# Performance work log

Hardware: AMD Instinct MI355X
Metric: run time of the kernel (lower is better)

## Reference

```python
import jax, jax.numpy as jnp
import numpy as np

N_HEAD = 8
D_ATTN = 64
D_MODEL = 512


def setup_inputs() -> dict:
    key = jax.random.key(0)
    ks = jax.random.split(key, 12)
    B, S = 2, 2048
    inp = {
        "input": jax.random.normal(ks[0], (B, S, D_MODEL), dtype=jnp.float32),
        "top": jax.random.normal(ks[1], (B, S, S, 16), dtype=jnp.float32),
        # learned params (Linear: y = x @ W.T + b)
        "top_w": jax.random.normal(ks[2], (1, 16), dtype=jnp.float32) * 0.25,
        "top_b": jnp.zeros((1,), dtype=jnp.float32),
        "wq": jax.random.normal(ks[3], (N_HEAD * D_ATTN, D_MODEL), dtype=jnp.float32) * 0.02,
        "bq": jnp.zeros((N_HEAD * D_ATTN,), dtype=jnp.float32),
        "wk": jax.random.normal(ks[4], (N_HEAD * D_ATTN, D_MODEL), dtype=jnp.float32) * 0.02,
        "bk": jnp.zeros((N_HEAD * D_ATTN,), dtype=jnp.float32),
        "wv": jax.random.normal(ks[5], (N_HEAD * D_ATTN, D_MODEL), dtype=jnp.float32) * 0.02,
        "bv": jnp.zeros((N_HEAD * D_ATTN,), dtype=jnp.float32),
        "wo": jax.random.normal(ks[6], (D_MODEL, N_HEAD * D_ATTN), dtype=jnp.float32) * 0.02,
        "bo": jnp.zeros((D_MODEL,), dtype=jnp.float32),
    }
    return inp


def reference(input, top, top_w, top_b, wq, bq, wk, bk, wv, bv, wo, bo):
    B, S, _ = input.shape
    # pairwise topological bias: [B,S,S,16] @ [16,1] -> [B,S,S]
    bias = (jnp.einsum('bstf,f->bst', top, top_w[0]) + top_b[0])  # [B,S,S]
    bias = bias[:, None, :, :]  # broadcast over heads: [B,1,S,S]

    def proj(w, b):
        # [B,S,D] -> [B,H,S,d]
        return (input @ w.T + b).reshape(B, S, N_HEAD, D_ATTN).transpose(0, 2, 1, 3)

    Q, K, V = proj(wq, bq), proj(wk, bk), proj(wv, bv)
    scores = jnp.einsum('bhqd,bhkd->bhqk', Q, K) / jnp.sqrt(jnp.float32(D_ATTN))
    attn = jax.nn.softmax(scores + bias, axis=-1)
    O = jnp.einsum('bhqk,bhkd->bhqd', attn, V)  # [B,H,S,d]
    O = O.transpose(0, 2, 1, 3).reshape(B, S, N_HEAD * D_ATTN)
    return O @ wo.T + bo
```

## Files before the change

kernel.cpp:

```cpp
#include <hip/hip_runtime.h>
#include <math.h>

#define S_LEN 2048
#define BATCH 2
#define NH 8
#define DH 64
#define DM 512

typedef __attribute__((ext_vector_type(8))) short short8;
typedef __attribute__((ext_vector_type(4))) float floatx4;

__device__ __forceinline__ unsigned short f2bf(float f) {
  union { float f; unsigned u; } v; v.f = f;
  unsigned r = v.u + 0x7FFFu + ((v.u >> 16) & 1u);
  return (unsigned short)(r >> 16);
}

__global__ __launch_bounds__(256) void cvt_f32_bf16(const float* __restrict__ src,
                                                    unsigned short* __restrict__ dst, int n4) {
  int i = blockIdx.x * blockDim.x + threadIdx.x;
  if (i < n4) {
    float4 f = ((const float4*)src)[i];
    ushort4 o;
    o.x = f2bf(f.x); o.y = f2bf(f.y); o.z = f2bf(f.z); o.w = f2bf(f.w);
    ((ushort4*)dst)[i] = o;
  }
}

__global__ __launch_bounds__(256) void bias_topo(const float* __restrict__ top,
                                                 const float* __restrict__ top_w,
                                                 const float* __restrict__ top_b,
                                                 float* __restrict__ bias) {
  size_t e = (size_t)blockIdx.x * blockDim.x + threadIdx.x;
  const float4* t = (const float4*)(top + e * 16);
  const float4* w = (const float4*)top_w;
  float acc = top_b[0];
#pragma unroll
  for (int j = 0; j < 4; j++) {
    float4 tv = t[j]; float4 wv = w[j];
    acc += tv.x * wv.x + tv.y * wv.y + tv.z * wv.z + tv.w * wv.w;
  }
  bias[e] = acc;
}

__global__ __launch_bounds__(256) void gemm_bt(const unsigned short* __restrict__ A,
                                               const unsigned short* __restrict__ W,
                                               const float* __restrict__ bias,
                                               void* __restrict__ out, int mode, float scale) {
  __shared__ unsigned short As[64][72];
  __shared__ unsigned short Ws[64][72];
  const int m0 = blockIdx.x * 64, n0 = blockIdx.y * 64;
  const int tid = threadIdx.x;
  const int w = tid >> 6, l = tid & 63;
  const int lr = l & 15, lg = l >> 4;

  floatx4 acc[4];
#pragma unroll
  for (int nb = 0; nb < 4; nb++)
#pragma unroll
    for (int i = 0; i < 4; i++) acc[nb][i] = 0.f;

  const int srow = tid >> 2;
  const int sseg = (tid & 3) * 16;

  for (int k0 = 0; k0 < 512; k0 += 64) {
    const unsigned short* ap = A + (size_t)(m0 + srow) * 512 + k0 + sseg;
    const unsigned short* wp = W + (size_t)(n0 + srow) * 512 + k0 + sseg;
    *(short8*)&As[srow][sseg]     = *(const short8*)ap;
    *(short8*)&As[srow][sseg + 8] = *(const short8*)(ap + 8);
    *(short8*)&Ws[srow][sseg]     = *(const short8*)wp;
    *(short8*)&Ws[srow][sseg + 8] = *(const short8*)(wp + 8);
    __syncthreads();
#pragma unroll
    for (int kk = 0; kk < 2; kk++) {
      short8 af = *(const short8*)&As[w * 16 + lr][kk * 32 + lg * 8];
#pragma unroll
      for (int nb = 0; nb < 4; nb++) {
        short8 bf = *(const short8*)&Ws[nb * 16 + lr][kk * 32 + lg * 8];
        acc[nb] = __builtin_amdgcn_mfma_f32_16x16x32_bf16(af, bf, acc[nb], 0, 0, 0);
      }
    }
    __syncthreads();
  }

#pragma unroll
  for (int nb = 0; nb < 4; nb++) {
    const int n = n0 + nb * 16 + lr;
    const float bv = bias[n];
#pragma unroll
    for (int i = 0; i < 4; i++) {
      const int m = m0 + w * 16 + lg * 4 + i;
      float v = (acc[nb][i] + bv) * scale;
      if (mode == 0) {
        ((float*)out)[(size_t)m * 512 + n] = v;
      } else {
        const int b = m >> 11, s = m & 2047;
        const int h = n >> 6, d = n & 63;
        unsigned short* o = (unsigned short*)out;
        if (mode == 1)
          o[((size_t)(b * 8 + h) * 2048 + s) * 64 + d] = f2bf(v);
        else
          o[((size_t)(b * 8 + h) * 64 + d) * 2048 + s] = f2bf(v);
      }
    }
  }
}

__global__ __launch_bounds__(256) void attn_kernel(const unsigned short* __restrict__ Qb,
                                                   const unsigned short* __restrict__ Kb,
                                                   const unsigned short* __restrict__ Vt,
                                                   const float* __restrict__ biasb,
                                                   unsigned short* __restrict__ Ob) {
  __shared__ unsigned short P[4][16][80];
  const int q0 = blockIdx.x * 64;
  const int bh = blockIdx.y;
  const int b = bh >> 3, h = bh & 7;
  const int tid = threadIdx.x;
  const int w = tid >> 6, l = tid & 63;
  const int lr = l & 15, lg = l >> 4;

  const unsigned short* Qh = Qb + (size_t)bh * S_LEN * DH;
  const unsigned short* Kh = Kb + (size_t)bh * S_LEN * DH;
  const unsigned short* Vh = Vt + (size_t)bh * DH * S_LEN;

  const int qrow = q0 + w * 16;
  short8 qf[2];
  qf[0] = *(const short8*)(Qh + (size_t)(qrow + lr) * DH + lg * 8);
  qf[1] = *(const short8*)(Qh + (size_t)(qrow + lr) * DH + 32 + lg * 8);

  float m_i[4], l_i[4];
  floatx4 o[4];
#pragma unroll
  for (int i = 0; i < 4; i++) { m_i[i] = -1e30f; l_i[i] = 0.f; }
#pragma unroll
  for (int nd = 0; nd < 4; nd++)
#pragma unroll
    for (int i = 0; i < 4; i++) o[nd][i] = 0.f;

  const float* brow = biasb + ((size_t)b * S_LEN + qrow) * S_LEN;
  const float LOG2E = 1.44269504088896f;

  for (int k0 = 0; k0 < S_LEN; k0 += 64) {
    floatx4 sa[4];
#pragma unroll
    for (int nb = 0; nb < 4; nb++)
#pragma unroll
      for (int i = 0; i < 4; i++) sa[nb][i] = 0.f;
#pragma unroll
    for (int kk = 0; kk < 2; kk++) {
#pragma unroll
      for (int nb = 0; nb < 4; nb++) {
        short8 kf = *(const short8*)(Kh + (size_t)(k0 + nb * 16 + lr) * DH + kk * 32 + lg * 8);
        sa[nb] = __builtin_amdgcn_mfma_f32_16x16x32_bf16(qf[kk], kf, sa[nb], 0, 0, 0);
      }
    }
    float p[4][4];
#pragma unroll
    for (int i = 0; i < 4; i++) {
#pragma unroll
      for (int nb = 0; nb < 4; nb++) {
        float bv = brow[(size_t)(lg * 4 + i) * S_LEN + k0 + nb * 16 + lr];
        p[nb][i] = sa[nb][i] + bv;
      }
      float mx = fmaxf(fmaxf(p[0][i], p[1][i]), fmaxf(p[2][i], p[3][i]));
      mx = fmaxf(mx, __shfl_xor(mx, 1));
      mx = fmaxf(mx, __shfl_xor(mx, 2));
      mx = fmaxf(mx, __shfl_xor(mx, 4));
      mx = fmaxf(mx, __shfl_xor(mx, 8));
      float mnew = fmaxf(m_i[i], mx);
      float alpha = exp2f((m_i[i] - mnew) * LOG2E);
      float rs = 0.f;
#pragma unroll
      for (int nb = 0; nb < 4; nb++) {
        p[nb][i] = exp2f((p[nb][i] - mnew) * LOG2E);
        rs += p[nb][i];
      }
      rs += __shfl_xor(rs, 1);
      rs += __shfl_xor(rs, 2);
      rs += __shfl_xor(rs, 4);
      rs += __shfl_xor(rs, 8);
      l_i[i] = l_i[i] * alpha + rs;
      m_i[i] = mnew;
#pragma unroll
      for (int nd = 0; nd < 4; nd++) o[nd][i] *= alpha;
    }
#pragma unroll
    for (int nb = 0; nb < 4; nb++)
#pragma unroll
      for (int i = 0; i < 4; i++)
        P[w][lg * 4 + i][nb * 16 + lr] = f2bf(p[nb][i]);
    __syncthreads();
#pragma unroll
    for (int ks = 0; ks < 2; ks++) {
      short8 pf = *(const short8*)&P[w][lr][ks * 32 + lg * 8];
#pragma unroll
      for (int nd = 0; nd < 4; nd++) {
        short8 vf = *(const short8*)(Vh + (size_t)(nd * 16 + lr) * S_LEN + k0 + ks * 32 + lg * 8);
        o[nd] = __builtin_amdgcn_mfma_f32_16x16x32_bf16(pf, vf, o[nd], 0, 0, 0);
      }
    }
    __syncthreads();
  }

#pragma unroll
  for (int i = 0; i < 4; i++) {
    const float inv = 1.0f / l_i[i];
    const int s = qrow + lg * 4 + i;
#pragma unroll
    for (int nd = 0; nd < 4; nd++)
      Ob[((size_t)b * S_LEN + s) * DM + h * DH + nd * 16 + lr] = f2bf(o[nd][i] * inv);
  }
}

extern "C" void kernel_launch(void* const* d_in, const int* in_sizes, int n_in,
                              void* d_out, int out_size, void* d_ws, size_t ws_size,
                              hipStream_t stream) {
  const float* input = (const float*)d_in[0];
  const float* top   = (const float*)d_in[1];
  const float* top_w = (const float*)d_in[2];
  const float* top_b = (const float*)d_in[3];
  const float* wq = (const float*)d_in[4];
  const float* bq = (const float*)d_in[5];
  const float* wk = (const float*)d_in[6];
  const float* bk = (const float*)d_in[7];
  const float* wv = (const float*)d_in[8];
  const float* bv = (const float*)d_in[9];
  const float* wo = (const float*)d_in[10];
  const float* bo = (const float*)d_in[11];

  char* ws = (char*)d_ws;
  float* bias_ws = (float*)ws;              ws += (size_t)BATCH * S_LEN * S_LEN * 4;
  unsigned short* in_bf = (unsigned short*)ws;  ws += (size_t)BATCH * S_LEN * DM * 2;
  unsigned short* wq_bf = (unsigned short*)ws;  ws += (size_t)DM * DM * 2;
  unsigned short* wk_bf = (unsigned short*)ws;  ws += (size_t)DM * DM * 2;
  unsigned short* wv_bf = (unsigned short*)ws;  ws += (size_t)DM * DM * 2;
  unsigned short* wo_bf = (unsigned short*)ws;  ws += (size_t)DM * DM * 2;
  unsigned short* qb  = (unsigned short*)ws;    ws += (size_t)BATCH * NH * S_LEN * DH * 2;
  unsigned short* kb  = (unsigned short*)ws;    ws += (size_t)BATCH * NH * S_LEN * DH * 2;
  unsigned short* vtb = (unsigned short*)ws;    ws += (size_t)BATCH * NH * S_LEN * DH * 2;
  unsigned short* ob  = (unsigned short*)ws;    ws += (size_t)BATCH * S_LEN * DM * 2;

  const int nIn4 = BATCH * S_LEN * DM / 4;
  const int nW4  = DM * DM / 4;
  cvt_f32_bf16<<<nIn4 / 256, 256, 0, stream>>>(input, in_bf, nIn4);
  cvt_f32_bf16<<<nW4 / 256, 256, 0, stream>>>(wq, wq_bf, nW4);
  cvt_f32_bf16<<<nW4 / 256, 256, 0, stream>>>(wk, wk_bf, nW4);
  cvt_f32_bf16<<<nW4 / 256, 256, 0, stream>>>(wv, wv_bf, nW4);
  cvt_f32_bf16<<<nW4 / 256, 256, 0, stream>>>(wo, wo_bf, nW4);

  bias_topo<<<(BATCH * S_LEN * S_LEN) / 256, 256, 0, stream>>>(top, top_w, top_b, bias_ws);

  dim3 gg(4096 / 64, 512 / 64);
  gemm_bt<<<gg, 256, 0, stream>>>(in_bf, wq_bf, bq, qb, 1, 0.125f);
  gemm_bt<<<gg, 256, 0, stream>>>(in_bf, wk_bf, bk, kb, 1, 1.0f);
  gemm_bt<<<gg, 256, 0, stream>>>(in_bf, wv_bf, bv, vtb, 2, 1.0f);

  attn_kernel<<<dim3(S_LEN / 64, BATCH * NH), 256, 0, stream>>>(qb, kb, vtb, bias_ws, ob);

  gemm_bt<<<gg, 256, 0, stream>>>(ob, wo_bf, bo, d_out, 0, 1.0f);
}
```

Measured before the change: 916.8 us.

## Transpose attention MFMA layout, vectorize bias loads, drop syncs, batch weight casts

The attention kernel swaps the MFMA operand order so each lane owns a single query row. Bias reads become contiguous float4 loads, the softmax reduction needs only two cross-lane shuffles, the P tile is written per warp without __syncthreads, and output stores are vectorized. The V-projection GEMM now stages its transposed tile through LDS to make coalesced 16-byte stores, and the four weight conversions are merged into one launch. Removing the block barrier depends on each warp touching only its own P slice, which relies on wave-level execution ordering between the LDS write and read.

```diff
diff --git a/kernel.cpp b/kernel.cpp
--- a/kernel.cpp
+++ b/kernel.cpp
@@ -25,6 +25,24 @@
     o.x = f2bf(f.x); o.y = f2bf(f.y); o.z = f2bf(f.z); o.w = f2bf(f.w);
     ((ushort4*)dst)[i] = o;
   }
+}
+
+__global__ __launch_bounds__(256) void cvt4_f32_bf16(const float* __restrict__ a, const float* __restrict__ b,
+                                                     const float* __restrict__ c, const float* __restrict__ d,
+                                                     unsigned short* __restrict__ oa, unsigned short* __restrict__ ob,
+                                                     unsigned short* __restrict__ oc, unsigned short* __restrict__ od) {
+  const float* src; unsigned short* dst;
+  switch (blockIdx.y) {
+    case 0: src = a; dst = oa; break;
+    case 1: src = b; dst = ob; break;
+    case 2: src = c; dst = oc; break;
+    default: src = d; dst = od; break;
+  }
+  int i = blockIdx.x * blockDim.x + threadIdx.x;
+  float4 f = ((const float4*)src)[i];
+  ushort4 o;
+  o.x = f2bf(f.x); o.y = f2bf(f.y); o.z = f2bf(f.z); o.w = f2bf(f.w);
+  ((ushort4*)dst)[i] = o;
 }
 
 __global__ __launch_bounds__(256) void bias_topo(const float* __restrict__ top,
@@ -83,6 +101,29 @@
     __syncthreads();
   }
 
+  if (mode == 2) {
+#pragma unroll
+    for (int nb = 0; nb < 4; nb++) {
+      const float bv = bias[n0 + nb * 16 + lr];
+      ushort4 pk;
+      pk.x = f2bf(acc[nb][0] + bv);
+      pk.y = f2bf(acc[nb][1] + bv);
+      pk.z = f2bf(acc[nb][2] + bv);
+      pk.w = f2bf(acc[nb][3] + bv);
+      *(ushort4*)&As[nb * 16 + lr][w * 16 + lg * 4] = pk;
+    }
+    __syncthreads();
+    const int b = m0 >> 11, s_base = m0 & 2047;
+    const int h = n0 >> 6;
+    unsigned short* outp = (unsigned short*)out + (size_t)(b * 8 + h) * DH * S_LEN;
+    const int row = tid >> 2, seg = (tid & 3) * 16;
+    short8 v0 = *(const short8*)&As[row][seg];
+    short8 v1 = *(const short8*)&As[row][seg + 8];
+    *(short8*)(outp + (size_t)row * S_LEN + s_base + seg)     = v0;
+    *(short8*)(outp + (size_t)row * S_LEN + s_base + seg + 8) = v1;
+    return;
+  }
+
 #pragma unroll
   for (int nb = 0; nb < 4; nb++) {
     const int n = n0 + nb * 16 + lr;
@@ -96,11 +137,7 @@
       } else {
         const int b = m >> 11, s = m & 2047;
         const int h = n >> 6, d = n & 63;
-        unsigned short* o = (unsigned short*)out;
-        if (mode == 1)
-          o[((size_t)(b * 8 + h) * 2048 + s) * 64 + d] = f2bf(v);
-        else
-          o[((size_t)(b * 8 + h) * 64 + d) * 2048 + s] = f2bf(v);
+        ((unsigned short*)out)[((size_t)(b * 8 + h) * 2048 + s) * 64 + d] = f2bf(v);
       }
     }
   }
@@ -111,7 +148,7 @@
                                                    const unsigned short* __restrict__ Vt,
                                                    const float* __restrict__ biasb,
                                                    unsigned short* __restrict__ Ob) {
-  __shared__ unsigned short P[4][16][80];
+  __shared__ unsigned short Ps[4][16][72];
   const int q0 = blockIdx.x * 64;
   const int bh = blockIdx.y;
   const int b = bh >> 3, h = bh & 7;
@@ -123,21 +160,19 @@
   const unsigned short* Kh = Kb + (size_t)bh * S_LEN * DH;
   const unsigned short* Vh = Vt + (size_t)bh * DH * S_LEN;
 
-  const int qrow = q0 + w * 16;
+  const int q = q0 + w * 16 + lr;
   short8 qf[2];
-  qf[0] = *(const short8*)(Qh + (size_t)(qrow + lr) * DH + lg * 8);
-  qf[1] = *(const short8*)(Qh + (size_t)(qrow + lr) * DH + 32 + lg * 8);
-
-  float m_i[4], l_i[4];
+  qf[0] = *(const short8*)(Qh + (size_t)q * DH + lg * 8);
+  qf[1] = *(const short8*)(Qh + (size_t)q * DH + 32 + lg * 8);
+
+  float m_i = -1e30f, l_i = 0.f;
   floatx4 o[4];
 #pragma unroll
-  for (int i = 0; i < 4; i++) { m_i[i] = -1e30f; l_i[i] = 0.f; }
-#pragma unroll
   for (int nd = 0; nd < 4; nd++)
 #pragma unroll
     for (int i = 0; i < 4; i++) o[nd][i] = 0.f;
 
-  const float* brow = biasb + ((size_t)b * S_LEN + qrow) * S_LEN;
+  const float* brow = biasb + ((size_t)b * S_LEN + q) * S_LEN;
   const float LOG2E = 1.44269504088896f;
 
   for (int k0 = 0; k0 < S_LEN; k0 += 64) {
@@ -151,64 +186,67 @@
 #pragma unroll
       for (int nb = 0; nb < 4; nb++) {
         short8 kf = *(const short8*)(Kh + (size_t)(k0 + nb * 16 + lr) * DH + kk * 32 + lg * 8);
-        sa[nb] = __builtin_amdgcn_mfma_f32_16x16x32_bf16(qf[kk], kf, sa[nb], 0, 0, 0);
+        sa[nb] = __builtin_amdgcn_mfma_f32_16x16x32_bf16(kf, qf[kk], sa[nb], 0, 0, 0);
       }
     }
     float p[4][4];
-#pragma unroll
-    for (int i = 0; i < 4; i++) {
-#pragma unroll
-      for (int nb = 0; nb < 4; nb++) {
-        float bv = brow[(size_t)(lg * 4 + i) * S_LEN + k0 + nb * 16 + lr];
-        p[nb][i] = sa[nb][i] + bv;
-      }
-      float mx = fmaxf(fmaxf(p[0][i], p[1][i]), fmaxf(p[2][i], p[3][i]));
-      mx = fmaxf(mx, __shfl_xor(mx, 1));
-      mx = fmaxf(mx, __shfl_xor(mx, 2));
-      mx = fmaxf(mx, __shfl_xor(mx, 4));
-      mx = fmaxf(mx, __shfl_xor(mx, 8));
-      float mnew = fmaxf(m_i[i], mx);
-      float alpha = exp2f((m_i[i] - mnew) * LOG2E);
-      float rs = 0.f;
-#pragma unroll
-      for (int nb = 0; nb < 4; nb++) {
+    float mx = -1e30f;
+#pragma unroll
+    for (int nb = 0; nb < 4; nb++) {
+      float4 bv = *(const float4*)(brow + k0 + nb * 16 + lg * 4);
+      p[nb][0] = sa[nb][0] + bv.x;
+      p[nb][1] = sa[nb][1] + bv.y;
+      p[nb][2] = sa[nb][2] + bv.z;
+      p[nb][3] = sa[nb][3] + bv.w;
+      mx = fmaxf(mx, fmaxf(fmaxf(p[nb][0], p[nb][1]), fmaxf(p[nb][2], p[nb][3])));
+    }
+    mx = fmaxf(mx, __shfl_xor(mx, 16));
+    mx = fmaxf(mx, __shfl_xor(mx, 32));
+    const float mnew = fmaxf(m_i, mx);
+    const float alpha = exp2f((m_i - mnew) * LOG2E);
+    float rs = 0.f;
+#pragma unroll
+    for (int nb = 0; nb < 4; nb++)
+#pragma unroll
+      for (int i = 0; i < 4; i++) {
         p[nb][i] = exp2f((p[nb][i] - mnew) * LOG2E);
         rs += p[nb][i];
       }
-      rs += __shfl_xor(rs, 1);
-      rs += __shfl_xor(rs, 2);
-      rs += __shfl_xor(rs, 4);
-      rs += __shfl_xor(rs, 8);
-      l_i[i] = l_i[i] * alpha + rs;
-      m_i[i] = mnew;
-#pragma unroll
-      for (int nd = 0; nd < 4; nd++) o[nd][i] *= alpha;
-    }
-#pragma unroll
-    for (int nb = 0; nb < 4; nb++)
-#pragma unroll
-      for (int i = 0; i < 4; i++)
-        P[w][lg * 4 + i][nb * 16 + lr] = f2bf(p[nb][i]);
-    __syncthreads();
-#pragma unroll
-    for (int ks = 0; ks < 2; ks++) {
-      short8 pf = *(const short8*)&P[w][lr][ks * 32 + lg * 8];
+    rs += __shfl_xor(rs, 16);
+    rs += __shfl_xor(rs, 32);
+    l_i = l_i * alpha + rs;
+    m_i = mnew;
+#pragma unroll
+    for (int nd = 0; nd < 4; nd++)
+#pragma unroll
+      for (int i = 0; i < 4; i++) o[nd][i] *= alpha;
+#pragma unroll
+    for (int nb = 0; nb < 4; nb++) {
+      ushort4 pk;
+      pk.x = f2bf(p[nb][0]); pk.y = f2bf(p[nb][1]);
+      pk.z = f2bf(p[nb][2]); pk.w = f2bf(p[nb][3]);
+      *(ushort4*)&Ps[w][lr][nb * 16 + lg * 4] = pk;
+    }
+#pragma unroll
+    for (int kk = 0; kk < 2; kk++) {
+      short8 pf = *(const short8*)&Ps[w][lr][kk * 32 + lg * 8];
 #pragma unroll
       for (int nd = 0; nd < 4; nd++) {
-        short8 vf = *(const short8*)(Vh + (size_t)(nd * 16 + lr) * S_LEN + k0 + ks * 32 + lg * 8);
-        o[nd] = __builtin_amdgcn_mfma_f32_16x16x32_bf16(pf, vf, o[nd], 0, 0, 0);
-      }
-    }
-    __syncthreads();
-  }
-
-#pragma unroll
-  for (int i = 0; i < 4; i++) {
-    const float inv = 1.0f / l_i[i];
-    const int s = qrow + lg * 4 + i;
-#pragma unroll
-    for (int nd = 0; nd < 4; nd++)
-      Ob[((size_t)b * S_LEN + s) * DM + h * DH + nd * 16 + lr] = f2bf(o[nd][i] * inv);
+        short8 vf = *(const short8*)(Vh + (size_t)(nd * 16 + lr) * S_LEN + k0 + kk * 32 + lg * 8);
+        o[nd] = __builtin_amdgcn_mfma_f32_16x16x32_bf16(vf, pf, o[nd], 0, 0, 0);
+      }
+    }
+  }
+
+  const float inv = 1.0f / l_i;
+#pragma unroll
+  for (int nd = 0; nd < 4; nd++) {
+    ushort4 st;
+    st.x = f2bf(o[nd][0] * inv);
+    st.y = f2bf(o[nd][1] * inv);
+    st.z = f2bf(o[nd][2] * inv);
+    st.w = f2bf(o[nd][3] * inv);
+    *(ushort4*)(Ob + ((size_t)b * S_LEN + q) * DM + h * DH + nd * 16 + lg * 4) = st;
   }
 }
 
@@ -243,10 +281,7 @@
   const int nIn4 = BATCH * S_LEN * DM / 4;
   const int nW4  = DM * DM / 4;
   cvt_f32_bf16<<<nIn4 / 256, 256, 0, stream>>>(input, in_bf, nIn4);
-  cvt_f32_bf16<<<nW4 / 256, 256, 0, stream>>>(wq, wq_bf, nW4);
-  cvt_f32_bf16<<<nW4 / 256, 256, 0, stream>>>(wk, wk_bf, nW4);
-  cvt_f32_bf16<<<nW4 / 256, 256, 0, stream>>>(wv, wv_bf, nW4);
-  cvt_f32_bf16<<<nW4 / 256, 256, 0, stream>>>(wo, wo_bf, nW4);
+  cvt4_f32_bf16<<<dim3(nW4 / 256, 4), 256, 0, stream>>>(wq, wk, wv, wo, wq_bf, wk_bf, wv_bf, wo_bf);
 
   bias_topo<<<(BATCH * S_LEN * S_LEN) / 256, 256, 0, stream>>>(top, top_w, top_b, bias_ws);
 
```

New measurement: 894.6 us. 1.02x faster.
